# Kernel tuning notes

Measured on AMD Instinct MI355X. Metric: run time of the kernel, lower is better.

Reference implementation:

```python
import jax, jax.numpy as jnp
import numpy as np

EPS = 1e-12  # torch F.normalize eps

def _l2norm(x):
    n = jnp.linalg.norm(x, axis=-1, keepdims=True)
    return x / jnp.maximum(n, EPS)

def setup_inputs() -> dict:
    key = jax.random.key(0)
    k0, k1, k2, k3 = jax.random.split(key, 4)
    B, S, L, E, N = 16, 2048, 512, 512, 2048
    z = jax.random.normal(k0, (B, S, L), dtype=jnp.float32)
    mask = jnp.ones((B, S), dtype=bool)  # unused by the module's forward body
    # learned params (xavier-ish scales)
    W_in = jax.random.normal(k1, (E, L), dtype=jnp.float32) / np.float32(np.sqrt(L))
    b_in = jnp.zeros((E,), dtype=jnp.float32)
    W_out = jax.random.normal(k2, (L, E), dtype=jnp.float32) / np.float32(np.sqrt(E))
    b_out = jnp.zeros((L,), dtype=jnp.float32)
    emb = jax.random.normal(k3, (N, E), dtype=jnp.float32) / np.float32(np.sqrt(E))
    return {"z": z, "mask": mask, "W_in": W_in, "b_in": b_in, "W_out": W_out, "b_out": b_out, "emb": emb}

def reference(z, mask, W_in, b_in, W_out, b_out, emb):
    B, S, L = z.shape
    zf = z.reshape(B * S, L)
    zf = zf @ W_in.T + b_in                 # (BS, E) input projection
    zf = _l2norm(zf)                        # F.normalize over dim=1
    emb_n = _l2norm(emb)                    # codebook rows normalized in-place in torch
    d = -(zf @ emb_n.T)                     # (BS, N) negative cosine similarity
    min_encoding_indices = jnp.argmin(d, axis=1)   # (BS,)
    zq = emb_n[min_encoding_indices]        # gather codebook vectors (BS, E)
    zq = zq @ W_out.T + b_out               # output projection (BS, L)
    zq = zq.reshape(B, S, L)
    zq = z + jax.lax.stop_gradient(zq - z)  # straight-through estimator
    return zq, min_encoding_indices
```

## Files before the change

### kernel.cpp

```cpp
#include <hip/hip_runtime.h>
#include <math.h>

#define BS_TOK 32768
#define DIM 512
#define NCODE 2048

typedef _Float16 f16x8 __attribute__((ext_vector_type(8)));
typedef _Float16 f16x4 __attribute__((ext_vector_type(4)));
typedef float f32x16 __attribute__((ext_vector_type(16)));

#define LDH 40

#define LGKM0_FENCE asm volatile("s_waitcnt lgkmcnt(0)" ::: "memory")
#define SBAR __builtin_amdgcn_s_barrier()

__global__ __launch_bounds__(256) void k_rownorm_split(
    const float* __restrict__ in, _Float16* __restrict__ hi,
    _Float16* __restrict__ lo, int rstride) {
  const int r = blockIdx.x;
  const int t = threadIdx.x;
  const float* row = in + (size_t)r * DIM;
  float v0 = row[t];
  float v1 = row[t + 256];
  float s = v0 * v0 + v1 * v1;
#pragma unroll
  for (int off = 32; off > 0; off >>= 1) s += __shfl_down(s, off, 64);
  __shared__ float ls[4];
  if ((t & 63) == 0) ls[t >> 6] = s;
  __syncthreads();
  float tot = ls[0] + ls[1] + ls[2] + ls[3];
  float sc = 1.0f / fmaxf(sqrtf(tot), 1e-12f);
  float x0 = v0 * sc, x1 = v1 * sc;
  _Float16 h0 = (_Float16)x0;
  _Float16 h1 = (_Float16)x1;
  _Float16 e0 = (_Float16)((x0 - (float)h0) * 2048.0f);
  _Float16 e1 = (_Float16)((x1 - (float)h1) * 2048.0f);
  _Float16* hrow = hi + (size_t)r * rstride;
  _Float16* lrow = lo + (size_t)r * rstride;
  hrow[t] = h0;
  hrow[t + 256] = h1;
  lrow[t] = e0;
  lrow[t + 256] = e1;
}

__global__ __launch_bounds__(256) void k_split_w(const float* __restrict__ w,
                                                 _Float16* __restrict__ hi,
                                                 _Float16* __restrict__ lo) {
  int t = (blockIdx.x * 256 + threadIdx.x) * 4;
  float4 v = *(const float4*)(w + t);
  f16x4 h, l;
  h.x = (_Float16)v.x; l.x = (_Float16)((v.x - (float)h.x) * 2048.0f);
  h.y = (_Float16)v.y; l.y = (_Float16)((v.y - (float)h.y) * 2048.0f);
  h.z = (_Float16)v.z; l.z = (_Float16)((v.z - (float)h.z) * 2048.0f);
  h.w = (_Float16)v.w; l.w = (_Float16)((v.w - (float)h.w) * 2048.0f);
  *(f16x4*)(hi + t) = h;
  *(f16x4*)(lo + t) = l;
}

__global__ __launch_bounds__(256, 2) void k_gemm_mfma_in(
    const float* __restrict__ A, const _Float16* __restrict__ Bhi,
    const _Float16* __restrict__ Blo, const float* __restrict__ bias,
    float* __restrict__ C) {
  __shared__ __align__(16) _Float16 sm[2][4][128 * LDH];
  const int tid = threadIdx.x;
  const int w = tid >> 6, l = tid & 63;
  const int wm = w >> 1, wn = w & 1;
  const int lm = l & 31, lh = l >> 5;
  const int m0 = blockIdx.y * 128;
  const int n0 = blockIdx.x * 128;
  const int arow = tid >> 3;
  const int ac4 = (tid & 7) << 2;
  const int brow = tid >> 2;
  const int bq = (tid & 3) << 3;

  f32x16 aHH[2][2], aX[2][2];
#pragma unroll
  for (int mb = 0; mb < 2; ++mb)
#pragma unroll
    for (int nb = 0; nb < 2; ++nb) {
      aHH[mb][nb] = (f32x16)0.0f;
      aX[mb][nb] = (f32x16)0.0f;
    }

  float4 ar[4];
  f16x8 brh[2], brl[2];

  auto LOADS = [&](int kt) {
#pragma unroll
    for (int i = 0; i < 4; ++i)
      ar[i] =
          *(const float4*)(A + (size_t)(m0 + arow + 32 * i) * DIM + kt * 32 + ac4);
#pragma unroll
    for (int i = 0; i < 2; ++i) {
      const size_t g = (size_t)(n0 + brow + 64 * i) * DIM + kt * 32 + bq;
      brh[i] = *(const f16x8*)(Bhi + g);
      brl[i] = *(const f16x8*)(Blo + g);
    }
  };
  auto WRITES = [&](int b) {
#pragma unroll
    for (int i = 0; i < 4; ++i) {
      f16x4 h, lo4;
      h.x = (_Float16)ar[i].x; lo4.x = (_Float16)((ar[i].x - (float)h.x) * 2048.0f);
      h.y = (_Float16)ar[i].y; lo4.y = (_Float16)((ar[i].y - (float)h.y) * 2048.0f);
      h.z = (_Float16)ar[i].z; lo4.z = (_Float16)((ar[i].z - (float)h.z) * 2048.0f);
      h.w = (_Float16)ar[i].w; lo4.w = (_Float16)((ar[i].w - (float)h.w) * 2048.0f);
      *(f16x4*)(&sm[b][0][(arow + 32 * i) * LDH + ac4]) = h;
      *(f16x4*)(&sm[b][1][(arow + 32 * i) * LDH + ac4]) = lo4;
    }
#pragma unroll
    for (int i = 0; i < 2; ++i) {
      *(f16x8*)(&sm[b][2][(brow + 64 * i) * LDH + bq]) = brh[i];
      *(f16x8*)(&sm[b][3][(brow + 64 * i) * LDH + bq]) = brl[i];
    }
  };

  LOADS(0);
  WRITES(0);
  LOADS(1);
  LGKM0_FENCE;
  SBAR;
  int cur = 0;
  const int NT = DIM / 32;
  for (int t = 0; t < NT; ++t) {
    if (t < NT - 1) WRITES(cur ^ 1);
    if (t < NT - 2) LOADS(t + 2);
#pragma unroll
    for (int c = 0; c < 2; ++c) {
      const int ko = c * 16 + lh * 8;
      f16x8 ah[2], al[2], bh[2], bl[2];
#pragma unroll
      for (int mb = 0; mb < 2; ++mb) {
        int r = wm * 64 + mb * 32 + lm;
        ah[mb] = *(const f16x8*)(&sm[cur][0][r * LDH + ko]);
        al[mb] = *(const f16x8*)(&sm[cur][1][r * LDH + ko]);
      }
#pragma unroll
      for (int nb = 0; nb < 2; ++nb) {
        int r = wn * 64 + nb * 32 + lm;
        bh[nb] = *(const f16x8*)(&sm[cur][2][r * LDH + ko]);
        bl[nb] = *(const f16x8*)(&sm[cur][3][r * LDH + ko]);
      }
#pragma unroll
      for (int mb = 0; mb < 2; ++mb)
#pragma unroll
        for (int nb = 0; nb < 2; ++nb) {
          aHH[mb][nb] = __builtin_amdgcn_mfma_f32_32x32x16_f16(
              ah[mb], bh[nb], aHH[mb][nb], 0, 0, 0);
          aX[mb][nb] = __builtin_amdgcn_mfma_f32_32x32x16_f16(
              ah[mb], bl[nb], aX[mb][nb], 0, 0, 0);
          aX[mb][nb] = __builtin_amdgcn_mfma_f32_32x32x16_f16(
              al[mb], bh[nb], aX[mb][nb], 0, 0, 0);
        }
    }
    LGKM0_FENCE;
    SBAR;
    cur ^= 1;
  }
#pragma unroll
  for (int nb = 0; nb < 2; ++nb) {
    int n = n0 + wn * 64 + nb * 32 + lm;
    float bv = bias[n];
#pragma unroll
    for (int mb = 0; mb < 2; ++mb)
#pragma unroll
      for (int r = 0; r < 16; ++r) {
        int m = m0 + wm * 64 + mb * 32 + (r & 3) + 8 * (r >> 2) + 4 * lh;
        C[(size_t)m * DIM + n] =
            aHH[mb][nb][r] + aX[mb][nb][r] * (1.0f / 2048.0f) + bv;
      }
  }
}

__global__ __launch_bounds__(256, 2) void k_gemm_mfma_gather(
    const _Float16* __restrict__ Ahi, const _Float16* __restrict__ Alo,
    const _Float16* __restrict__ Bhi, const _Float16* __restrict__ Blo,
    const float* __restrict__ bias, float* __restrict__ C,
    const int* __restrict__ gather, const float* __restrict__ zin) {
  __shared__ __align__(16) _Float16 sm[2][4][128 * LDH];
  const int tid = threadIdx.x;
  const int w = tid >> 6, l = tid & 63;
  const int wm = w >> 1, wn = w & 1;
  const int lm = l & 31, lh = l >> 5;
  const int m0 = blockIdx.y * 128;
  const int n0 = blockIdx.x * 128;
  const int brow = tid >> 2;
  const int bq = (tid & 3) << 3;
  const size_t g0 = (size_t)gather[m0 + brow] * DIM;
  const size_t g1 = (size_t)gather[m0 + 64 + brow] * DIM;

  f32x16 aHH[2][2], aX[2][2];
#pragma unroll
  for (int mb = 0; mb < 2; ++mb)
#pragma unroll
    for (int nb = 0; nb < 2; ++nb) {
      aHH[mb][nb] = (f32x16)0.0f;
      aX[mb][nb] = (f32x16)0.0f;
    }

  f16x8 arh[2], arl[2], brh[2], brl[2];

  auto LOADS = [&](int kt) {
    const int kc = kt * 32 + bq;
    arh[0] = *(const f16x8*)(Ahi + g0 + kc);
    arl[0] = *(const f16x8*)(Alo + g0 + kc);
    arh[1] = *(const f16x8*)(Ahi + g1 + kc);
    arl[1] = *(const f16x8*)(Alo + g1 + kc);
#pragma unroll
    for (int i = 0; i < 2; ++i) {
      const size_t g = (size_t)(n0 + brow + 64 * i) * DIM + kc;
      brh[i] = *(const f16x8*)(Bhi + g);
      brl[i] = *(const f16x8*)(Blo + g);
    }
  };
  auto WRITES = [&](int b) {
#pragma unroll
    for (int i = 0; i < 2; ++i) {
      *(f16x8*)(&sm[b][0][(brow + 64 * i) * LDH + bq]) = arh[i];
      *(f16x8*)(&sm[b][1][(brow + 64 * i) * LDH + bq]) = arl[i];
      *(f16x8*)(&sm[b][2][(brow + 64 * i) * LDH + bq]) = brh[i];
      *(f16x8*)(&sm[b][3][(brow + 64 * i) * LDH + bq]) = brl[i];
    }
  };

  LOADS(0);
  WRITES(0);
  LOADS(1);
  LGKM0_FENCE;
  SBAR;
  int cur = 0;
  const int NT = DIM / 32;
  for (int t = 0; t < NT; ++t) {
    if (t < NT - 1) WRITES(cur ^ 1);
    if (t < NT - 2) LOADS(t + 2);
#pragma unroll
    for (int c = 0; c < 2; ++c) {
      const int ko = c * 16 + lh * 8;
      f16x8 ah[2], al[2], bh[2], bl[2];
#pragma unroll
      for (int mb = 0; mb < 2; ++mb) {
        int r = wm * 64 + mb * 32 + lm;
        ah[mb] = *(const f16x8*)(&sm[cur][0][r * LDH + ko]);
        al[mb] = *(const f16x8*)(&sm[cur][1][r * LDH + ko]);
      }
#pragma unroll
      for (int nb = 0; nb < 2; ++nb) {
        int r = wn * 64 + nb * 32 + lm;
        bh[nb] = *(const f16x8*)(&sm[cur][2][r * LDH + ko]);
        bl[nb] = *(const f16x8*)(&sm[cur][3][r * LDH + ko]);
      }
#pragma unroll
      for (int mb = 0; mb < 2; ++mb)
#pragma unroll
        for (int nb = 0; nb < 2; ++nb) {
          aHH[mb][nb] = __builtin_amdgcn_mfma_f32_32x32x16_f16(
              ah[mb], bh[nb], aHH[mb][nb], 0, 0, 0);
          aX[mb][nb] = __builtin_amdgcn_mfma_f32_32x32x16_f16(
              ah[mb], bl[nb], aX[mb][nb], 0, 0, 0);
          aX[mb][nb] = __builtin_amdgcn_mfma_f32_32x32x16_f16(
              al[mb], bh[nb], aX[mb][nb], 0, 0, 0);
        }
    }
    LGKM0_FENCE;
    SBAR;
    cur ^= 1;
  }
#pragma unroll
  for (int nb = 0; nb < 2; ++nb) {
    int n = n0 + wn * 64 + nb * 32 + lm;
    float bv = bias[n];
#pragma unroll
    for (int mb = 0; mb < 2; ++mb)
#pragma unroll
      for (int r = 0; r < 16; ++r) {
        int m = m0 + wm * 64 + mb * 32 + (r & 3) + 8 * (r >> 2) + 4 * lh;
        float val = aHH[mb][nb][r] + aX[mb][nb][r] * (1.0f / 2048.0f) + bv;
        float zv = zin[(size_t)m * DIM + n];
        C[(size_t)m * DIM + n] = zv + (val - zv);
      }
  }
}

#define SIMK_BM 128
#define SIMK_BN 128
#define NQUART 4
#define QCODES (NCODE / NQUART)

__global__ __launch_bounds__(256, 4) void k_sim_argmax(
    const _Float16* __restrict__ Apack,
    const _Float16* __restrict__ Bhi, unsigned* __restrict__ cand) {
  __shared__ __align__(16) _Float16 sm[2][2][128 * LDH];
  float* sC = (float*)sm;

  const int tid = threadIdx.x;
  const int w = tid >> 6, l = tid & 63;
  const int wm = w >> 1, wn = w & 1;
  const int lm = l & 31, lh = l >> 5;
  const int q = blockIdx.x & (NQUART - 1);
  const int tokbase = (blockIdx.x >> 2) * SIMK_BM;
  const int code0 = q * QCODES;
  const int brow = tid >> 2;
  const int bq = (tid & 3) << 3;
  const int t_red = tid >> 1, h_red = tid & 1;

  unsigned e0 = 0, e1 = 0, e2 = 0, e3 = 0;

  f16x8 arh[2], brh[2];

  auto LOADS = [&](int nt, int kt) {
    const int kc = kt * 32 + bq;
#pragma unroll
    for (int i = 0; i < 2; ++i) {
      arh[i] =
          *(const f16x8*)(Apack + (size_t)(tokbase + brow + 64 * i) * 1024 + kc);
      brh[i] =
          *(const f16x8*)(Bhi + (size_t)(code0 + nt + brow + 64 * i) * DIM + kc);
    }
  };
  auto WRITES = [&](int b) {
#pragma unroll
    for (int i = 0; i < 2; ++i) {
      *(f16x8*)(&sm[b][0][(brow + 64 * i) * LDH + bq]) = arh[i];
      *(f16x8*)(&sm[b][1][(brow + 64 * i) * LDH + bq]) = brh[i];
    }
  };

  for (int nt = 0; nt < QCODES; nt += SIMK_BN) {
    f32x16 aHH[2][2];
#pragma unroll
    for (int mb = 0; mb < 2; ++mb)
#pragma unroll
      for (int nb = 0; nb < 2; ++nb) aHH[mb][nb] = (f32x16)0.0f;
    __syncthreads();
    LOADS(nt, 0);
    WRITES(0);
    LOADS(nt, 1);
    LGKM0_FENCE;
    SBAR;
    int cur = 0;
    for (int t = 0; t < 16; ++t) {
      if (t < 15) WRITES(cur ^ 1);
      if (t < 14) LOADS(nt, t + 2);
#pragma unroll
      for (int c = 0; c < 2; ++c) {
        const int ko = c * 16 + lh * 8;
        f16x8 ah[2], bh[2];
#pragma unroll
        for (int mb = 0; mb < 2; ++mb)
          ah[mb] = *(const f16x8*)(&sm[cur][0][(wm * 64 + mb * 32 + lm) * LDH + ko]);
#pragma unroll
        for (int nb = 0; nb < 2; ++nb)
          bh[nb] = *(const f16x8*)(&sm[cur][1][(wn * 64 + nb * 32 + lm) * LDH + ko]);
#pragma unroll
        for (int mb = 0; mb < 2; ++mb)
#pragma unroll
          for (int nb = 0; nb < 2; ++nb)
            aHH[mb][nb] = __builtin_amdgcn_mfma_f32_32x32x16_f16(
                ah[mb], bh[nb], aHH[mb][nb], 0, 0, 0);
      }
      LGKM0_FENCE;
      SBAR;
      cur ^= 1;
    }
#pragma unroll
    for (int p = 0; p < 2; ++p) {
      __syncthreads();
      if (wn == p) {
#pragma unroll
        for (int mb = 0; mb < 2; ++mb)
#pragma unroll
          for (int nb = 0; nb < 2; ++nb) {
            int nl = nb * 32 + lm;
#pragma unroll
            for (int r = 0; r < 16; ++r) {
              int m = wm * 64 + mb * 32 + (r & 3) + 8 * (r >> 2) + 4 * lh;
              sC[m * 65 + nl] = aHH[mb][nb][r];
            }
          }
      }
      __syncthreads();
      const float* rowp = &sC[t_red * 65 + h_red * 32];
      const int ncomp = 2047 - (code0 + nt + p * 64 + h_red * 32);
#pragma unroll
      for (int i = 0; i < 32; ++i) {
        float v = rowp[i];
        unsigned s = __float_as_uint(v);
        s = (s & 0x80000000u) ? ~s : (s | 0x80000000u);
        unsigned key = (s & 0xFFFFF800u) | (unsigned)(ncomp - i);
        if (key > e3) {
          unsigned y = key, t2;
          t2 = e0 > y ? e0 : y; y = e0 > y ? y : e0; e0 = t2;
          t2 = e1 > y ? e1 : y; y = e1 > y ? y : e1; e1 = t2;
          t2 = e2 > y ? e2 : y; y = e2 > y ? y : e2; e2 = t2;
          e3 = e3 > y ? e3 : y;
        }
      }
    }
  }
  unsigned o0 = __shfl_xor(e0, 1), o1 = __shfl_xor(e1, 1),
           o2 = __shfl_xor(e2, 1), o3 = __shfl_xor(e3, 1);
#define INS4(x)                                    \
  {                                                \
    unsigned y = (x), t2;                          \
    t2 = e0 > y ? e0 : y; y = e0 > y ? y : e0; e0 = t2; \
    t2 = e1 > y ? e1 : y; y = e1 > y ? y : e1; e1 = t2; \
    t2 = e2 > y ? e2 : y; y = e2 > y ? y : e2; e2 = t2; \
    e3 = e3 > y ? e3 : y;                          \
  }
  INS4(o0) INS4(o1) INS4(o2) INS4(o3)
  if (h_red == 0) {
    unsigned* cp = cand + ((size_t)(tokbase + t_red) * NQUART + q) * 4;
    cp[0] = e0; cp[1] = e1; cp[2] = e2; cp[3] = e3;
  }
}

#define THETA 2.125e-3f

__global__ __launch_bounds__(256) void k_refine(
    const unsigned* __restrict__ cand, const _Float16* __restrict__ zf16,
    const _Float16* __restrict__ embhi, const _Float16* __restrict__ emblo,
    int* __restrict__ idx, float* __restrict__ idxf) {
  const int tok = (blockIdx.x << 2) + (threadIdx.x >> 6);
  const int lane = threadIdx.x & 63;
  unsigned k32 = (lane < 16) ? cand[(size_t)tok * 16 + lane] : 0u;
  unsigned m1 = k32, m2 = 0;
#pragma unroll
  for (int off = 1; off < 64; off <<= 1) {
    unsigned q1 = __shfl_xor(m1, off), q2 = __shfl_xor(m2, off);
    unsigned hi = m1 > q1 ? m1 : q1;
    unsigned lo = m1 > q1 ? q1 : m1;
    unsigned s2 = m2 > q2 ? m2 : q2;
    m2 = lo > s2 ? lo : s2;
    m1 = hi;
  }
  unsigned s1 = m1 & 0xFFFFF800u, s2e = m2 & 0xFFFFF800u;
  float v1 = __uint_as_float((s1 & 0x80000000u) ? (s1 & 0x7FFFFFFFu) : ~s1);
  float v2 = __uint_as_float((s2e & 0x80000000u) ? (s2e & 0x7FFFFFFFu) : ~s2e);
  if (v1 - v2 >= THETA) {
    if (lane == 0) {
      int n1 = 2047 - (int)(m1 & 0x7FFu);
      idx[tok] = n1;
      idxf[tok] = (float)n1;
    }
    return;
  }
  const int c = lane & 15, seg = lane >> 4;
  unsigned ck = __shfl(k32, c);
  int n = 2047 - (int)(ck & 0x7FFu);
  const _Float16* zh = zf16 + (size_t)tok * 1024 + seg * 128;
  const _Float16* eh = embhi + (size_t)n * DIM + seg * 128;
  const _Float16* el = emblo + (size_t)n * DIM + seg * 128;
  float s = 0.0f;
#pragma unroll
  for (int d = 0; d < 128; d += 8) {
    f16x8 a = *(const f16x8*)(zh + d);
    f16x8 b = *(const f16x8*)(zh + 512 + d);
    f16x8 e = *(const f16x8*)(eh + d);
    f16x8 f = *(const f16x8*)(el + d);
#pragma unroll
    for (int j = 0; j < 8; ++j)
      s += ((float)a[j] + (float)b[j] * (1.0f / 2048.0f)) *
           ((float)e[j] + (float)f[j] * (1.0f / 2048.0f));
  }
  s += __shfl_xor(s, 16);
  s += __shfl_xor(s, 32);
  unsigned sb = __float_as_uint(s);
  sb = (sb & 0x80000000u) ? ~sb : (sb | 0x80000000u);
  unsigned long long kk =
      ((unsigned long long)sb << 32) | (unsigned)(2047 - n);
  if (lane >= 16) kk = 0ull;
#pragma unroll
  for (int off = 1; off < 16; off <<= 1) {
    unsigned long long o = __shfl_xor(kk, off);
    kk = o > kk ? o : kk;
  }
  if (lane == 0) {
    int nb = 2047 - (int)((unsigned)kk & 0x7FFu);
    idx[tok] = nb;
    idxf[tok] = (float)nb;
  }
}

extern "C" void kernel_launch(void* const* d_in, const int* in_sizes, int n_in,
                              void* d_out, int out_size, void* d_ws,
                              size_t ws_size, hipStream_t stream) {
  const float* z = (const float*)d_in[0];
  const float* W_in = (const float*)d_in[2];
  const float* b_in = (const float*)d_in[3];
  const float* W_out = (const float*)d_in[4];
  const float* b_out = (const float*)d_in[5];
  const float* emb = (const float*)d_in[6];

  float* out = (float*)d_out;
  float* zq = out;
  float* idxf = out + (size_t)BS_TOK * DIM;

  _Float16* embhi = (_Float16*)d_ws;
  _Float16* emblo = embhi + (size_t)NCODE * DIM;
  _Float16* winhi = emblo + (size_t)NCODE * DIM;
  _Float16* winlo = winhi + (size_t)DIM * DIM;
  _Float16* wouthi = winlo + (size_t)DIM * DIM;
  _Float16* woutlo = wouthi + (size_t)DIM * DIM;
  unsigned* cand = (unsigned*)(woutlo + (size_t)DIM * DIM);
  int* idx = (int*)(cand + (size_t)BS_TOK * 16);

  float* zf = zq;
  _Float16* zf16 = (_Float16*)zf;

  k_split_w<<<DIM * DIM / 1024, 256, 0, stream>>>(W_in, winhi, winlo);
  k_split_w<<<DIM * DIM / 1024, 256, 0, stream>>>(W_out, wouthi, woutlo);
  k_rownorm_split<<<NCODE, 256, 0, stream>>>(emb, embhi, emblo, DIM);
  k_gemm_mfma_in<<<dim3(DIM / 128, BS_TOK / 128), 256, 0, stream>>>(
      z, winhi, winlo, b_in, zf);
  k_rownorm_split<<<BS_TOK, 256, 0, stream>>>(zf, zf16, zf16 + 512, 1024);
  k_sim_argmax<<<(BS_TOK / SIMK_BM) * NQUART, 256, 0, stream>>>(zf16, embhi,
                                                                cand);
  k_refine<<<BS_TOK / 4, 256, 0, stream>>>(cand, zf16, embhi, emblo, idx,
                                           idxf);
  k_gemm_mfma_gather<<<dim3(DIM / 128, BS_TOK / 128), 256, 0, stream>>>(
      embhi, emblo, wouthi, woutlo, b_out, zq, idx, z);
}
```

Before: 425.4 us.

## Precompute projected codebook table and gather; skip token normalization

The output projection now runs once over the 2048 normalized codebook rows into a table. A simple gather kernel then applies the straight-through expression per token, replacing the 32768-row gathered GEMM. The input projection writes split fp16 hi/lo values directly and drops the per-token row normalization pass, since argmax is scale-invariant. The refine threshold becomes relative to the token norm to account for the unnormalized similarities. This trades precision-threshold tuning risk for removing a large GEMM and a full normalization pass.

```diff
diff --git a/kernel.cpp b/kernel.cpp
--- a/kernel.cpp
+++ b/kernel.cpp
@@ -60,7 +60,7 @@
 __global__ __launch_bounds__(256, 2) void k_gemm_mfma_in(
     const float* __restrict__ A, const _Float16* __restrict__ Bhi,
     const _Float16* __restrict__ Blo, const float* __restrict__ bias,
-    float* __restrict__ C) {
+    _Float16* __restrict__ zf16) {
   __shared__ __align__(16) _Float16 sm[2][4][128 * LDH];
   const int tid = threadIdx.x;
   const int w = tid >> 6, l = tid & 63;
@@ -166,17 +166,19 @@
 #pragma unroll
       for (int r = 0; r < 16; ++r) {
         int m = m0 + wm * 64 + mb * 32 + (r & 3) + 8 * (r >> 2) + 4 * lh;
-        C[(size_t)m * DIM + n] =
-            aHH[mb][nb][r] + aX[mb][nb][r] * (1.0f / 2048.0f) + bv;
-      }
-  }
-}
-
-__global__ __launch_bounds__(256, 2) void k_gemm_mfma_gather(
+        float val = aHH[mb][nb][r] + aX[mb][nb][r] * (1.0f / 2048.0f) + bv;
+        _Float16 h = (_Float16)val;
+        _Float16 lo = (_Float16)((val - (float)h) * 2048.0f);
+        zf16[(size_t)m * 1024 + n] = h;
+        zf16[(size_t)m * 1024 + 512 + n] = lo;
+      }
+  }
+}
+
+__global__ __launch_bounds__(256, 2) void k_gemm_codebook(
     const _Float16* __restrict__ Ahi, const _Float16* __restrict__ Alo,
     const _Float16* __restrict__ Bhi, const _Float16* __restrict__ Blo,
-    const float* __restrict__ bias, float* __restrict__ C,
-    const int* __restrict__ gather, const float* __restrict__ zin) {
+    const float* __restrict__ bias, float* __restrict__ table) {
   __shared__ __align__(16) _Float16 sm[2][4][128 * LDH];
   const int tid = threadIdx.x;
   const int w = tid >> 6, l = tid & 63;
@@ -186,8 +188,6 @@
   const int n0 = blockIdx.x * 128;
   const int brow = tid >> 2;
   const int bq = (tid & 3) << 3;
-  const size_t g0 = (size_t)gather[m0 + brow] * DIM;
-  const size_t g1 = (size_t)gather[m0 + 64 + brow] * DIM;
 
   f32x16 aHH[2][2], aX[2][2];
 #pragma unroll
@@ -202,12 +202,11 @@
 
   auto LOADS = [&](int kt) {
     const int kc = kt * 32 + bq;
-    arh[0] = *(const f16x8*)(Ahi + g0 + kc);
-    arl[0] = *(const f16x8*)(Alo + g0 + kc);
-    arh[1] = *(const f16x8*)(Ahi + g1 + kc);
-    arl[1] = *(const f16x8*)(Alo + g1 + kc);
 #pragma unroll
     for (int i = 0; i < 2; ++i) {
+      const size_t ga = (size_t)(m0 + brow + 64 * i) * DIM + kc;
+      arh[i] = *(const f16x8*)(Ahi + ga);
+      arl[i] = *(const f16x8*)(Alo + ga);
       const size_t g = (size_t)(n0 + brow + 64 * i) * DIM + kc;
       brh[i] = *(const f16x8*)(Bhi + g);
       brl[i] = *(const f16x8*)(Blo + g);
@@ -274,11 +273,27 @@
 #pragma unroll
       for (int r = 0; r < 16; ++r) {
         int m = m0 + wm * 64 + mb * 32 + (r & 3) + 8 * (r >> 2) + 4 * lh;
-        float val = aHH[mb][nb][r] + aX[mb][nb][r] * (1.0f / 2048.0f) + bv;
-        float zv = zin[(size_t)m * DIM + n];
-        C[(size_t)m * DIM + n] = zv + (val - zv);
-      }
-  }
+        table[(size_t)m * DIM + n] =
+            aHH[mb][nb][r] + aX[mb][nb][r] * (1.0f / 2048.0f) + bv;
+      }
+  }
+}
+
+__global__ __launch_bounds__(256) void k_gather_st(
+    const float* __restrict__ z, const float* __restrict__ table,
+    const int* __restrict__ idx, float* __restrict__ out) {
+  int g = blockIdx.x * 256 + threadIdx.x;
+  int m = g >> 7;
+  int c = (g & 127) << 2;
+  int n = idx[m];
+  float4 t = *(const float4*)(table + (size_t)n * DIM + c);
+  float4 zv = *(const float4*)(z + (size_t)m * DIM + c);
+  float4 o;
+  o.x = zv.x + (t.x - zv.x);
+  o.y = zv.y + (t.y - zv.y);
+  o.z = zv.z + (t.z - zv.z);
+  o.w = zv.w + (t.w - zv.w);
+  *(float4*)(out + (size_t)m * DIM + c) = o;
 }
 
 #define SIMK_BM 128
@@ -414,14 +429,22 @@
   }
 }
 
-#define THETA 2.125e-3f
-
 __global__ __launch_bounds__(256) void k_refine(
     const unsigned* __restrict__ cand, const _Float16* __restrict__ zf16,
     const _Float16* __restrict__ embhi, const _Float16* __restrict__ emblo,
     int* __restrict__ idx, float* __restrict__ idxf) {
   const int tok = (blockIdx.x << 2) + (threadIdx.x >> 6);
   const int lane = threadIdx.x & 63;
+  f16x8 zh8 = *(const f16x8*)(zf16 + (size_t)tok * 1024 + lane * 8);
+  float ss = 0.0f;
+#pragma unroll
+  for (int j = 0; j < 8; ++j) {
+    float x = (float)zh8[j];
+    ss += x * x;
+  }
+#pragma unroll
+  for (int off = 1; off < 64; off <<= 1) ss += __shfl_xor(ss, off);
+
   unsigned k32 = (lane < 16) ? cand[(size_t)tok * 16 + lane] : 0u;
   unsigned m1 = k32, m2 = 0;
 #pragma unroll
@@ -436,7 +459,9 @@
   unsigned s1 = m1 & 0xFFFFF800u, s2e = m2 & 0xFFFFF800u;
   float v1 = __uint_as_float((s1 & 0x80000000u) ? (s1 & 0x7FFFFFFFu) : ~s1);
   float v2 = __uint_as_float((s2e & 0x80000000u) ? (s2e & 0x7FFFFFFFu) : ~s2e);
-  if (v1 - v2 >= THETA) {
+  float theta = 2.0e-3f * sqrtf(ss) +
+                9.765625e-4f * (fabsf(v1) + fabsf(v2)) + 1e-6f;
+  if (v1 - v2 >= theta) {
     if (lane == 0) {
       int n1 = 2047 - (int)(m1 & 0x7FFu);
       idx[tok] = n1;
@@ -501,22 +526,23 @@
   _Float16* winlo = winhi + (size_t)DIM * DIM;
   _Float16* wouthi = winlo + (size_t)DIM * DIM;
   _Float16* woutlo = wouthi + (size_t)DIM * DIM;
-  unsigned* cand = (unsigned*)(woutlo + (size_t)DIM * DIM);
-  int* idx = (int*)(cand + (size_t)BS_TOK * 16);
-
-  float* zf = zq;
-  _Float16* zf16 = (_Float16*)zf;
+  int* idx = (int*)(woutlo + (size_t)DIM * DIM);
+  unsigned* cand = (unsigned*)(idx + BS_TOK);
+  float* table = (float*)cand;
+
+  _Float16* zf16 = (_Float16*)zq;
 
   k_split_w<<<DIM * DIM / 1024, 256, 0, stream>>>(W_in, winhi, winlo);
   k_split_w<<<DIM * DIM / 1024, 256, 0, stream>>>(W_out, wouthi, woutlo);
   k_rownorm_split<<<NCODE, 256, 0, stream>>>(emb, embhi, emblo, DIM);
   k_gemm_mfma_in<<<dim3(DIM / 128, BS_TOK / 128), 256, 0, stream>>>(
-      z, winhi, winlo, b_in, zf);
-  k_rownorm_split<<<BS_TOK, 256, 0, stream>>>(zf, zf16, zf16 + 512, 1024);
+      z, winhi, winlo, b_in, zf16);
   k_sim_argmax<<<(BS_TOK / SIMK_BM) * NQUART, 256, 0, stream>>>(zf16, embhi,
                                                                 cand);
   k_refine<<<BS_TOK / 4, 256, 0, stream>>>(cand, zf16, embhi, emblo, idx,
                                            idxf);
-  k_gemm_mfma_gather<<<dim3(DIM / 128, BS_TOK / 128), 256, 0, stream>>>(
-      embhi, emblo, wouthi, woutlo, b_out, zq, idx, z);
-}
+  k_gemm_codebook<<<dim3(DIM / 128, NCODE / 128), 256, 0, stream>>>(
+      embhi, emblo, wouthi, woutlo, b_out, table);
+  k_gather_st<<<BS_TOK * (DIM / 4) / 256, 256, 0, stream>>>(z, table, idx,
+                                                            zq);
+}
```

Result: faster. 392.5 us (-7.7%).
